# Kernel tuning notes

Measured on AMD Instinct MI355X. Metric: run time of the kernel, lower is better.

## Reference

```python
import jax, jax.numpy as jnp
import numpy as np

DEPTH = 4  # truncation depth of the signature


def setup_inputs() -> dict:
    key = jax.random.key(0)
    # (N, L, C) batch of paths
    path = jax.random.normal(key, (64, 512, 8), dtype=jnp.float32)
    return {"path": path}


def _signature(path, depth):
    """Truncated path signature: exp(dx_1) (x) exp(dx_2) (x) ... via Chen's relation.

    Signature state is kept as a tuple of flattened tensor levels, level k has
    shape (N, C**k). Combining a signature S with exp(z) gives, at level k:
        sum_{j=0}^{k} S_{k-j} (x) z^{(x)j} / j!   (with S_0 = 1)
    """
    N, L, C = path.shape
    # increments, scanned over the stream dim: (L-1, N, C)
    diffs = jnp.swapaxes(path[:, 1:] - path[:, :-1], 0, 1)

    def step(sig, z):
        # powers[j-1] = z^{(x)j} / j!, flattened to (N, C**j)
        powers = [z]
        for j in range(2, depth + 1):
            powers.append((powers[-1][:, :, None] * z[:, None, :]).reshape(N, -1) / j)
        new = []
        for k in range(1, depth + 1):
            term = sig[k - 1] + powers[k - 1]  # j=0 and j=k terms
            for j in range(1, k):
                # S_{k-j} (x) z^{(x)j}/j!
                term = term + (sig[k - j - 1][:, :, None]
                               * powers[j - 1][:, None, :]).reshape(N, C ** k)
            new.append(term)
        return tuple(new), None

    # identity element of the tensor algebra: all levels >= 1 are zero
    init = tuple(jnp.zeros((N, C ** k), dtype=path.dtype) for k in range(1, depth + 1))
    sig, _ = jax.lax.scan(step, init, diffs)
    # (N, C + C^2 + ... + C^depth)
    return jnp.concatenate(sig, axis=-1)


def reference(path) -> jnp.ndarray:
    return _signature(path, DEPTH)
```

## Files before the change

### kernel.cpp

```cpp
#include <hip/hip_runtime.h>


#define NB 64
#define LP 512
#define SIG 4680
#define O2 8
#define O3 72
#define O4 584
#define L123_F4 146

__device__ __forceinline__ void prod_core(
    float (&a4)[16], const float (&b4)[16],
    const float* Ap, float* Aq, const float* B,
    int tid, int w, int l, int a, int b)
{
    const int c0 = 2 * w;
    const float A1   = Ap[a];
    const float A2   = Ap[O2 + a * 8 + b];
    const float A3_0 = Ap[O3 + (a * 8 + b) * 8 + c0];
    const float A3_1 = Ap[O3 + (a * 8 + b) * 8 + c0 + 1];
    float b1[8];
    *(float4*)&b1[0] = *(const float4*)(B);
    *(float4*)&b1[4] = *(const float4*)(B + 4);
    float b2r[16], b3r[16];
    #pragma unroll
    for (int i = 0; i < 4; ++i) {
        *(float4*)&b2r[4 * i] = *(const float4*)(B + O2 + c0 * 8 + 4 * i);
        *(float4*)&b3r[4 * i] = *(const float4*)(B + O3 + (b * 8 + c0) * 8 + 4 * i);
    }
    #pragma unroll
    for (int cc = 0; cc < 2; ++cc) {
        const float A3c = cc ? A3_1 : A3_0;
        #pragma unroll
        for (int d = 0; d < 8; ++d)
            a4[cc * 8 + d] += b4[cc * 8 + d] + A3c * b1[d]
                            + A2 * b2r[cc * 8 + d] + A1 * b3r[cc * 8 + d];
    }
    const int f0 = 2 * tid;
    const int pp = f0 >> 6, qq = (f0 >> 3) & 7, rr = f0 & 7;
    const float A1p  = Ap[pp];
    const float A2pq = Ap[O2 + pp * 8 + qq];
    Aq[O3 + f0]     = Ap[O3 + f0]     + B[O3 + f0]
                    + A2pq * B[rr]     + A1p * B[O2 + qq * 8 + rr];
    Aq[O3 + f0 + 1] = Ap[O3 + f0 + 1] + B[O3 + f0 + 1]
                    + A2pq * B[rr + 1] + A1p * B[O2 + qq * 8 + rr + 1];
    if (tid < 64) Aq[O2 + tid] = Ap[O2 + tid] + B[O2 + tid] + Ap[tid >> 3] * B[tid & 7];
    if (tid < 8)  Aq[tid] = Ap[tid] + B[tid];
}

__global__ __launch_bounds__(256) void k1_sig4(const float* __restrict__ path,
                                               float* __restrict__ ws)
{
    __shared__ __align__(16) float zbuf[128 * 8];
    __shared__ __align__(16) float sL[4][584];
    __shared__ float4 sT[4][1024];
    __shared__ __align__(16) float sA[2][584];

    const int tid = threadIdx.x;
    const int n = blockIdx.x >> 2;
    const int g = blockIdx.x & 3;

    {
        const int r = tid >> 1, h = tid & 1;
        const int t = g * 128 + r;
        const float4* p4 = (const float4*)path + (size_t)n * (LP * 2);
        float4 z4 = make_float4(0.f, 0.f, 0.f, 0.f);
        if (t < LP - 1) {
            float4 x0 = p4[t * 2 + h];
            float4 x1 = p4[t * 2 + 2 + h];
            z4 = make_float4(x1.x - x0.x, x1.y - x0.y, x1.z - x0.z, x1.w - x0.w);
        }
        ((float4*)zbuf)[tid] = z4;
    }
    __syncthreads();

    const int w = tid >> 6, l = tid & 63;
    const int a = l >> 3, b = l & 7;

    float s1 = 0.f, s2 = 0.f, s3[8], s4[64];
    #pragma unroll
    for (int c = 0; c < 8; ++c) s3[c] = 0.f;
    #pragma unroll
    for (int e = 0; e < 64; ++e) s4[e] = 0.f;

    const float* zw = zbuf + w * (32 * 8);
    #pragma unroll 4
    for (int s = 0; s < 32; ++s) {
        const float* zs = zw + s * 8;
        float z[8];
        float4 zl = ((const float4*)zs)[0];
        float4 zh = ((const float4*)zs)[1];
        z[0]=zl.x; z[1]=zl.y; z[2]=zl.z; z[3]=zl.w;
        z[4]=zh.x; z[5]=zh.y; z[6]=zh.z; z[7]=zh.w;
        const float za  = zs[a];
        const float zbv = zs[b];
        const float B4 = zbv * (za * (1.f/24.f) + s1 * (1.f/6.f)) + s2 * 0.5f;
        const float G3 = zbv * (za * (1.f/6.f)  + s1 * 0.5f)      + s2;
        #pragma unroll
        for (int c = 0; c < 8; ++c) {
            const float Ac = B4 * z[c] + s3[c];
            #pragma unroll
            for (int d = 0; d < 8; ++d) s4[c*8+d] += Ac * z[d];
            s3[c] += G3 * z[c];
        }
        s2 += zbv * (za * 0.5f + s1);
        s1 += za;
    }

    if (b == 0) sL[w][a] = s1;
    sL[w][O2 + l] = s2;
    *(float4*)&sL[w][O3 + l * 8]     = make_float4(s3[0], s3[1], s3[2], s3[3]);
    *(float4*)&sL[w][O3 + l * 8 + 4] = make_float4(s3[4], s3[5], s3[6], s3[7]);
    #pragma unroll
    for (int i = 0; i < 16; ++i)
        sT[w][i * 64 + l] = make_float4(s4[4*i], s4[4*i+1], s4[4*i+2], s4[4*i+3]);
    __syncthreads();

    float a4[16], b4[16];
    #pragma unroll
    for (int k = 0; k < 4; ++k) {
        float4 v = sT[0][(w * 4 + k) * 64 + l];
        a4[4*k] = v.x; a4[4*k+1] = v.y; a4[4*k+2] = v.z; a4[4*k+3] = v.w;
    }
    #pragma unroll
    for (int k = 0; k < 4; ++k) {
        float4 v = sT[1][(w * 4 + k) * 64 + l];
        b4[4*k] = v.x; b4[4*k+1] = v.y; b4[4*k+2] = v.z; b4[4*k+3] = v.w;
    }
    prod_core(a4, b4, sL[0], sA[0], sL[1], tid, w, l, a, b);
    __syncthreads();
    #pragma unroll
    for (int k = 0; k < 4; ++k) {
        float4 v = sT[2][(w * 4 + k) * 64 + l];
        b4[4*k] = v.x; b4[4*k+1] = v.y; b4[4*k+2] = v.z; b4[4*k+3] = v.w;
    }
    prod_core(a4, b4, sA[0], sA[1], sL[2], tid, w, l, a, b);
    __syncthreads();
    #pragma unroll
    for (int k = 0; k < 4; ++k) {
        float4 v = sT[3][(w * 4 + k) * 64 + l];
        b4[4*k] = v.x; b4[4*k+1] = v.y; b4[4*k+2] = v.z; b4[4*k+3] = v.w;
    }
    prod_core(a4, b4, sA[1], sA[0], sL[3], tid, w, l, a, b);
    __syncthreads();

    float* dst = ws + (size_t)blockIdx.x * SIG;
    if (tid < L123_F4) ((float4*)dst)[tid] = ((const float4*)sA[0])[tid];
    float4* dT = (float4*)(dst + O4);
    #pragma unroll
    for (int k = 0; k < 4; ++k)
        dT[(w * 4 + k) * 64 + l] = make_float4(a4[4*k], a4[4*k+1], a4[4*k+2], a4[4*k+3]);
}

__global__ __launch_bounds__(256) void k2_final(const float* __restrict__ ws,
                                                float* __restrict__ out)
{
    __shared__ __align__(16) float sL[4][584];
    __shared__ __align__(16) float sA[2][584];

    const int tid = threadIdx.x;
    const int n = blockIdx.x;
    const int w = tid >> 6, l = tid & 63;
    const int a = l >> 3, b = l & 7;
    const float* base = ws + (size_t)n * 4 * SIG;

    #pragma unroll
    for (int s = 0; s < 4; ++s)
        if (tid < L123_F4)
            ((float4*)sL[s])[tid] = ((const float4*)(base + (size_t)s * SIG))[tid];

    float a4[16], rb1[16], rb2[16], rb3[16];
    #pragma unroll
    for (int k = 0; k < 4; ++k) {
        const int ti = (w * 4 + k) * 64 + l;
        float4 v0 = ((const float4*)(base + O4))[ti];
        float4 v1 = ((const float4*)(base + SIG + O4))[ti];
        float4 v2 = ((const float4*)(base + 2 * SIG + O4))[ti];
        float4 v3 = ((const float4*)(base + 3 * SIG + O4))[ti];
        a4[4*k]=v0.x; a4[4*k+1]=v0.y; a4[4*k+2]=v0.z; a4[4*k+3]=v0.w;
        rb1[4*k]=v1.x; rb1[4*k+1]=v1.y; rb1[4*k+2]=v1.z; rb1[4*k+3]=v1.w;
        rb2[4*k]=v2.x; rb2[4*k+1]=v2.y; rb2[4*k+2]=v2.z; rb2[4*k+3]=v2.w;
        rb3[4*k]=v3.x; rb3[4*k+1]=v3.y; rb3[4*k+2]=v3.z; rb3[4*k+3]=v3.w;
    }
    __syncthreads();

    prod_core(a4, rb1, sL[0], sA[0], sL[1], tid, w, l, a, b);
    __syncthreads();
    prod_core(a4, rb2, sA[0], sA[1], sL[2], tid, w, l, a, b);
    __syncthreads();
    prod_core(a4, rb3, sA[1], sA[0], sL[3], tid, w, l, a, b);
    __syncthreads();

    float* dst = out + (size_t)n * SIG;
    if (tid < L123_F4) ((float4*)dst)[tid] = ((const float4*)sA[0])[tid];
    float4* d4 = (float4*)(dst + O4);
    #pragma unroll
    for (int k = 0; k < 4; ++k)
        d4[l * 16 + w * 4 + k] = make_float4(a4[4*k], a4[4*k+1], a4[4*k+2], a4[4*k+3]);
}

extern "C" void kernel_launch(void* const* d_in, const int* in_sizes, int n_in,
                              void* d_out, int out_size, void* d_ws, size_t ws_size,
                              hipStream_t stream) {
    const float* path = (const float*)d_in[0];
    float* out = (float*)d_out;
    float* ws  = (float*)d_ws;

    k1_sig4<<<NB * 4, 256, 0, stream>>>(path, ws);
    k2_final<<<NB, 256, 0, stream>>>(ws, out);
}
```

Measured before the change: 19.93 us.

## Split stream into eight chunks per path and pad level-3 shared layout

The first kernel now uses eight blocks per path, each handling 64 increments, so 512 blocks run instead of 256 and each wave's serial scan is halved. Level-4 tiles are staged through two reused shared buffers, which cuts the first kernel's shared memory. Level-3 data in shared memory is padded (stride 9 for A, 72-per-row for B) to reduce bank conflicts. The final kernel must now combine eight partial signatures instead of four, with seven serial products and the next tile's global loads issued before each product, which lengthens that kernel's critical path.

```diff
diff --git a/kernel.cpp b/kernel.cpp
--- a/kernel.cpp
+++ b/kernel.cpp
@@ -7,7 +7,11 @@
 #define O2 8
 #define O3 72
 #define O4 584
+#define SB 648
 #define L123_F4 146
+
+#define A3IDX(pq, r) (72 + (pq) * 9 + (r))
+#define B3IDX(x, y, z) (72 + (x) * 72 + (y) * 8 + (z))
 
 __device__ __forceinline__ void prod_core(
     float (&a4)[16], const float (&b4)[16],
@@ -17,8 +21,8 @@
     const int c0 = 2 * w;
     const float A1   = Ap[a];
     const float A2   = Ap[O2 + a * 8 + b];
-    const float A3_0 = Ap[O3 + (a * 8 + b) * 8 + c0];
-    const float A3_1 = Ap[O3 + (a * 8 + b) * 8 + c0 + 1];
+    const float A3_0 = Ap[A3IDX(a * 8 + b, c0)];
+    const float A3_1 = Ap[A3IDX(a * 8 + b, c0 + 1)];
     float b1[8];
     *(float4*)&b1[0] = *(const float4*)(B);
     *(float4*)&b1[4] = *(const float4*)(B + 4);
@@ -26,7 +30,7 @@
     #pragma unroll
     for (int i = 0; i < 4; ++i) {
         *(float4*)&b2r[4 * i] = *(const float4*)(B + O2 + c0 * 8 + 4 * i);
-        *(float4*)&b3r[4 * i] = *(const float4*)(B + O3 + (b * 8 + c0) * 8 + 4 * i);
+        *(float4*)&b3r[4 * i] = *(const float4*)(B + B3IDX(b, c0, 0) + 4 * i);
     }
     #pragma unroll
     for (int cc = 0; cc < 2; ++cc) {
@@ -40,29 +44,29 @@
     const int pp = f0 >> 6, qq = (f0 >> 3) & 7, rr = f0 & 7;
     const float A1p  = Ap[pp];
     const float A2pq = Ap[O2 + pp * 8 + qq];
-    Aq[O3 + f0]     = Ap[O3 + f0]     + B[O3 + f0]
-                    + A2pq * B[rr]     + A1p * B[O2 + qq * 8 + rr];
-    Aq[O3 + f0 + 1] = Ap[O3 + f0 + 1] + B[O3 + f0 + 1]
-                    + A2pq * B[rr + 1] + A1p * B[O2 + qq * 8 + rr + 1];
+    Aq[A3IDX(pp * 8 + qq, rr)]     = Ap[A3IDX(pp * 8 + qq, rr)]
+        + B[B3IDX(pp, qq, rr)]     + A2pq * B[rr]     + A1p * B[O2 + qq * 8 + rr];
+    Aq[A3IDX(pp * 8 + qq, rr + 1)] = Ap[A3IDX(pp * 8 + qq, rr + 1)]
+        + B[B3IDX(pp, qq, rr + 1)] + A2pq * B[rr + 1] + A1p * B[O2 + qq * 8 + rr + 1];
     if (tid < 64) Aq[O2 + tid] = Ap[O2 + tid] + B[O2 + tid] + Ap[tid >> 3] * B[tid & 7];
     if (tid < 8)  Aq[tid] = Ap[tid] + B[tid];
 }
 
-__global__ __launch_bounds__(256) void k1_sig4(const float* __restrict__ path,
-                                               float* __restrict__ ws)
+__global__ __launch_bounds__(256) void k1_sig(const float* __restrict__ path,
+                                              float* __restrict__ ws)
 {
-    __shared__ __align__(16) float zbuf[128 * 8];
-    __shared__ __align__(16) float sL[4][584];
-    __shared__ float4 sT[4][1024];
-    __shared__ __align__(16) float sA[2][584];
+    __shared__ __align__(16) float zbuf[64 * 8];
+    __shared__ __align__(16) float sA[2][SB];
+    __shared__ __align__(16) float sL1[SB], sL2[SB], sL3[SB];
+    __shared__ __align__(16) float4 sTA[1024], sTB[1024];
 
     const int tid = threadIdx.x;
-    const int n = blockIdx.x >> 2;
-    const int g = blockIdx.x & 3;
-
-    {
+    const int n = blockIdx.x >> 3;
+    const int g = blockIdx.x & 7;
+
+    if (tid < 128) {
         const int r = tid >> 1, h = tid & 1;
-        const int t = g * 128 + r;
+        const int t = g * 64 + r;
         const float4* p4 = (const float4*)path + (size_t)n * (LP * 2);
         float4 z4 = make_float4(0.f, 0.f, 0.f, 0.f);
         if (t < LP - 1) {
@@ -76,6 +80,7 @@
 
     const int w = tid >> 6, l = tid & 63;
     const int a = l >> 3, b = l & 7;
+    const int f0 = 2 * tid;
 
     float s1 = 0.f, s2 = 0.f, s3[8], s4[64];
     #pragma unroll
@@ -83,9 +88,9 @@
     #pragma unroll
     for (int e = 0; e < 64; ++e) s4[e] = 0.f;
 
-    const float* zw = zbuf + w * (32 * 8);
+    const float* zw = zbuf + w * (16 * 8);
     #pragma unroll 4
-    for (int s = 0; s < 32; ++s) {
+    for (int s = 0; s < 16; ++s) {
         const float* zs = zw + s * 8;
         float z[8];
         float4 zl = ((const float4*)zs)[0];
@@ -107,45 +112,69 @@
         s1 += za;
     }
 
-    if (b == 0) sL[w][a] = s1;
-    sL[w][O2 + l] = s2;
-    *(float4*)&sL[w][O3 + l * 8]     = make_float4(s3[0], s3[1], s3[2], s3[3]);
-    *(float4*)&sL[w][O3 + l * 8 + 4] = make_float4(s3[4], s3[5], s3[6], s3[7]);
-    #pragma unroll
-    for (int i = 0; i < 16; ++i)
-        sT[w][i * 64 + l] = make_float4(s4[4*i], s4[4*i+1], s4[4*i+2], s4[4*i+3]);
+    if (w == 0) {
+        if (b == 0) sA[0][a] = s1;
+        sA[0][O2 + l] = s2;
+        #pragma unroll
+        for (int c = 0; c < 8; ++c) sA[0][A3IDX(l, c)] = s3[c];
+        #pragma unroll
+        for (int i = 0; i < 16; ++i)
+            sTA[i * 64 + l] = make_float4(s4[4*i], s4[4*i+1], s4[4*i+2], s4[4*i+3]);
+    } else {
+        float* SL = (w == 1) ? sL1 : (w == 2) ? sL2 : sL3;
+        if (b == 0) SL[a] = s1;
+        SL[O2 + l] = s2;
+        *(float4*)&SL[B3IDX(a, b, 0)] = make_float4(s3[0], s3[1], s3[2], s3[3]);
+        *(float4*)&SL[B3IDX(a, b, 4)] = make_float4(s3[4], s3[5], s3[6], s3[7]);
+        if (w == 1) {
+            #pragma unroll
+            for (int i = 0; i < 16; ++i)
+                sTB[i * 64 + l] = make_float4(s4[4*i], s4[4*i+1], s4[4*i+2], s4[4*i+3]);
+        }
+    }
     __syncthreads();
 
     float a4[16], b4[16];
     #pragma unroll
     for (int k = 0; k < 4; ++k) {
-        float4 v = sT[0][(w * 4 + k) * 64 + l];
-        a4[4*k] = v.x; a4[4*k+1] = v.y; a4[4*k+2] = v.z; a4[4*k+3] = v.w;
-    }
-    #pragma unroll
-    for (int k = 0; k < 4; ++k) {
-        float4 v = sT[1][(w * 4 + k) * 64 + l];
-        b4[4*k] = v.x; b4[4*k+1] = v.y; b4[4*k+2] = v.z; b4[4*k+3] = v.w;
-    }
-    prod_core(a4, b4, sL[0], sA[0], sL[1], tid, w, l, a, b);
-    __syncthreads();
-    #pragma unroll
-    for (int k = 0; k < 4; ++k) {
-        float4 v = sT[2][(w * 4 + k) * 64 + l];
-        b4[4*k] = v.x; b4[4*k+1] = v.y; b4[4*k+2] = v.z; b4[4*k+3] = v.w;
-    }
-    prod_core(a4, b4, sA[0], sA[1], sL[2], tid, w, l, a, b);
-    __syncthreads();
-    #pragma unroll
-    for (int k = 0; k < 4; ++k) {
-        float4 v = sT[3][(w * 4 + k) * 64 + l];
-        b4[4*k] = v.x; b4[4*k+1] = v.y; b4[4*k+2] = v.z; b4[4*k+3] = v.w;
-    }
-    prod_core(a4, b4, sA[1], sA[0], sL[3], tid, w, l, a, b);
+        float4 v = sTA[(w * 4 + k) * 64 + l];
+        a4[4*k]=v.x; a4[4*k+1]=v.y; a4[4*k+2]=v.z; a4[4*k+3]=v.w;
+        float4 u = sTB[(w * 4 + k) * 64 + l];
+        b4[4*k]=u.x; b4[4*k+1]=u.y; b4[4*k+2]=u.z; b4[4*k+3]=u.w;
+    }
+    prod_core(a4, b4, sA[0], sA[1], sL1, tid, w, l, a, b);
+    __syncthreads();
+    if (w == 2) {
+        #pragma unroll
+        for (int i = 0; i < 16; ++i)
+            sTA[i * 64 + l] = make_float4(s4[4*i], s4[4*i+1], s4[4*i+2], s4[4*i+3]);
+    }
+    __syncthreads();
+    #pragma unroll
+    for (int k = 0; k < 4; ++k) {
+        float4 u = sTA[(w * 4 + k) * 64 + l];
+        b4[4*k]=u.x; b4[4*k+1]=u.y; b4[4*k+2]=u.z; b4[4*k+3]=u.w;
+    }
+    prod_core(a4, b4, sA[1], sA[0], sL2, tid, w, l, a, b);
+    __syncthreads();
+    if (w == 3) {
+        #pragma unroll
+        for (int i = 0; i < 16; ++i)
+            sTB[i * 64 + l] = make_float4(s4[4*i], s4[4*i+1], s4[4*i+2], s4[4*i+3]);
+    }
+    __syncthreads();
+    #pragma unroll
+    for (int k = 0; k < 4; ++k) {
+        float4 u = sTB[(w * 4 + k) * 64 + l];
+        b4[4*k]=u.x; b4[4*k+1]=u.y; b4[4*k+2]=u.z; b4[4*k+3]=u.w;
+    }
+    prod_core(a4, b4, sA[0], sA[1], sL3, tid, w, l, a, b);
     __syncthreads();
 
     float* dst = ws + (size_t)blockIdx.x * SIG;
-    if (tid < L123_F4) ((float4*)dst)[tid] = ((const float4*)sA[0])[tid];
+    if (tid < O3) dst[tid] = sA[1][tid];
+    dst[O3 + f0]     = sA[1][A3IDX(f0 >> 3, f0 & 7)];
+    dst[O3 + f0 + 1] = sA[1][A3IDX(f0 >> 3, (f0 & 7) + 1)];
     float4* dT = (float4*)(dst + O4);
     #pragma unroll
     for (int k = 0; k < 4; ++k)
@@ -155,48 +184,64 @@
 __global__ __launch_bounds__(256) void k2_final(const float* __restrict__ ws,
                                                 float* __restrict__ out)
 {
-    __shared__ __align__(16) float sL[4][584];
-    __shared__ __align__(16) float sA[2][584];
+    __shared__ __align__(16) float sA[2][SB];
+    __shared__ __align__(16) float sLb[7][SB];
 
     const int tid = threadIdx.x;
     const int n = blockIdx.x;
     const int w = tid >> 6, l = tid & 63;
     const int a = l >> 3, b = l & 7;
-    const float* base = ws + (size_t)n * 4 * SIG;
-
-    #pragma unroll
-    for (int s = 0; s < 4; ++s)
-        if (tid < L123_F4)
-            ((float4*)sL[s])[tid] = ((const float4*)(base + (size_t)s * SIG))[tid];
-
-    float a4[16], rb1[16], rb2[16], rb3[16];
+    const int f0 = 2 * tid;
+    const float* base = ws + (size_t)n * 8 * SIG;
+
+    if (tid < O3) sA[0][tid] = base[tid];
+    sA[0][A3IDX(f0 >> 3, f0 & 7)]       = base[O3 + f0];
+    sA[0][A3IDX(f0 >> 3, (f0 & 7) + 1)] = base[O3 + f0 + 1];
+    #pragma unroll
+    for (int m = 1; m <= 7; ++m) {
+        if (tid < L123_F4) {
+            float4 v = ((const float4*)(base + (size_t)m * SIG))[tid];
+            int d4;
+            if (tid < 18) d4 = tid;
+            else { const int j = tid - 18; d4 = 18 + (j >> 4) * 18 + (j & 15); }
+            ((float4*)sLb[m - 1])[d4] = v;
+        }
+    }
+    float a4[16], b4A[16], b4B[16];
     #pragma unroll
     for (int k = 0; k < 4; ++k) {
         const int ti = (w * 4 + k) * 64 + l;
-        float4 v0 = ((const float4*)(base + O4))[ti];
-        float4 v1 = ((const float4*)(base + SIG + O4))[ti];
-        float4 v2 = ((const float4*)(base + 2 * SIG + O4))[ti];
-        float4 v3 = ((const float4*)(base + 3 * SIG + O4))[ti];
-        a4[4*k]=v0.x; a4[4*k+1]=v0.y; a4[4*k+2]=v0.z; a4[4*k+3]=v0.w;
-        rb1[4*k]=v1.x; rb1[4*k+1]=v1.y; rb1[4*k+2]=v1.z; rb1[4*k+3]=v1.w;
-        rb2[4*k]=v2.x; rb2[4*k+1]=v2.y; rb2[4*k+2]=v2.z; rb2[4*k+3]=v2.w;
-        rb3[4*k]=v3.x; rb3[4*k+1]=v3.y; rb3[4*k+2]=v3.z; rb3[4*k+3]=v3.w;
-    }
-    __syncthreads();
-
-    prod_core(a4, rb1, sL[0], sA[0], sL[1], tid, w, l, a, b);
-    __syncthreads();
-    prod_core(a4, rb2, sA[0], sA[1], sL[2], tid, w, l, a, b);
-    __syncthreads();
-    prod_core(a4, rb3, sA[1], sA[0], sL[3], tid, w, l, a, b);
-    __syncthreads();
+        float4 v = ((const float4*)(base + O4))[ti];
+        a4[4*k]=v.x; a4[4*k+1]=v.y; a4[4*k+2]=v.z; a4[4*k+3]=v.w;
+        float4 u = ((const float4*)(base + SIG + O4))[ti];
+        b4A[4*k]=u.x; b4A[4*k+1]=u.y; b4A[4*k+2]=u.z; b4A[4*k+3]=u.w;
+    }
+    __syncthreads();
+
+    #define LOADB4(dstv, mm)                                                   \
+        { _Pragma("unroll")                                                    \
+          for (int k = 0; k < 4; ++k) {                                        \
+              float4 u = ((const float4*)(base + (size_t)(mm) * SIG + O4))     \
+                             [(w * 4 + k) * 64 + l];                           \
+              dstv[4*k]=u.x; dstv[4*k+1]=u.y; dstv[4*k+2]=u.z; dstv[4*k+3]=u.w;\
+          } }
+
+    LOADB4(b4B, 2); prod_core(a4, b4A, sA[0], sA[1], sLb[0], tid, w, l, a, b); __syncthreads();
+    LOADB4(b4A, 3); prod_core(a4, b4B, sA[1], sA[0], sLb[1], tid, w, l, a, b); __syncthreads();
+    LOADB4(b4B, 4); prod_core(a4, b4A, sA[0], sA[1], sLb[2], tid, w, l, a, b); __syncthreads();
+    LOADB4(b4A, 5); prod_core(a4, b4B, sA[1], sA[0], sLb[3], tid, w, l, a, b); __syncthreads();
+    LOADB4(b4B, 6); prod_core(a4, b4A, sA[0], sA[1], sLb[4], tid, w, l, a, b); __syncthreads();
+    LOADB4(b4A, 7); prod_core(a4, b4B, sA[1], sA[0], sLb[5], tid, w, l, a, b); __syncthreads();
+                    prod_core(a4, b4A, sA[0], sA[1], sLb[6], tid, w, l, a, b); __syncthreads();
 
     float* dst = out + (size_t)n * SIG;
-    if (tid < L123_F4) ((float4*)dst)[tid] = ((const float4*)sA[0])[tid];
-    float4* d4 = (float4*)(dst + O4);
+    if (tid < O3) dst[tid] = sA[1][tid];
+    dst[O3 + f0]     = sA[1][A3IDX(f0 >> 3, f0 & 7)];
+    dst[O3 + f0 + 1] = sA[1][A3IDX(f0 >> 3, (f0 & 7) + 1)];
+    float4* d4p = (float4*)(dst + O4);
     #pragma unroll
     for (int k = 0; k < 4; ++k)
-        d4[l * 16 + w * 4 + k] = make_float4(a4[4*k], a4[4*k+1], a4[4*k+2], a4[4*k+3]);
+        d4p[l * 16 + w * 4 + k] = make_float4(a4[4*k], a4[4*k+1], a4[4*k+2], a4[4*k+3]);
 }
 
 extern "C" void kernel_launch(void* const* d_in, const int* in_sizes, int n_in,
@@ -206,6 +251,6 @@
     float* out = (float*)d_out;
     float* ws  = (float*)d_ws;
 
-    k1_sig4<<<NB * 4, 256, 0, stream>>>(path, ws);
+    k1_sig<<<NB * 8, 256, 0, stream>>>(path, ws);
     k2_final<<<NB, 256, 0, stream>>>(ws, out);
 }
```

After: 21.64 us. 1.09x slower.
